# Kernel tuning notes

Hardware: AMD Instinct MI355X
Metric: run time of the kernel (lower is better)

## Reference

```python
import jax, jax.numpy as jnp
import numpy as np

B, D, K = 16384, 256, 1024

def setup_inputs() -> dict:
    key = jax.random.key(0)
    k1, k2 = jax.random.split(key)
    x = jax.random.normal(k1, (B, D), dtype=jnp.float32)
    centers = jax.random.uniform(k2, (K, D), dtype=jnp.float32)  # RandomUniform(0,1)
    betas = jnp.ones((K,), dtype=jnp.float32)
    return {"x": x, "centers": centers, "betas": betas}

def reference(x, centers, betas):
    x_sq = jnp.sum(x * x, axis=-1, keepdims=True)          # [B,1]
    c_sq = jnp.sum(centers * centers, axis=-1)             # [K]
    cross = jnp.einsum('bd,kd->bk', x, centers)            # [B,K]
    diffnorm = x_sq + c_sq[None, :] - 2.0 * cross          # [B,K]
    return jnp.exp(-betas[None, :] * diffnorm)             # [B,K]
```

## Files before the change

kernel.cpp:

```cpp
#include <hip/hip_runtime.h>
#include <stdint.h>

#define D_DIM 256
#define K_CTR 1024
#define B_ROWS 16384
#define BM 32

typedef float f32x4 __attribute__((ext_vector_type(4)));
typedef long long i64x2 __attribute__((ext_vector_type(2)));

static __device__ __forceinline__ unsigned cvt4_fp8(const float4 v) {
    int r = __builtin_amdgcn_cvt_pk_fp8_f32(v.x, v.y, 0, false);
    r = __builtin_amdgcn_cvt_pk_fp8_f32(v.z, v.w, r, true);
    return (unsigned)r;
}

__global__ __launch_bounds__(256) void rbf_prep(const float* __restrict__ centers,
                                                unsigned char* __restrict__ cbf,
                                                float* __restrict__ csq) {
    const int w = threadIdx.x >> 6;
    const int l = threadIdx.x & 63;
    const int c0 = blockIdx.x * 4 + w;
    const float4 v = *reinterpret_cast<const float4*>(centers + c0 * D_DIM + l * 4);
    float s = v.x * v.x + v.y * v.y + v.z * v.z + v.w * v.w;
    const unsigned u = cvt4_fp8(v);
    const unsigned off = (unsigned)((c0 >> 4) * 4096 + (l >> 4) * 1024
                       + (((l >> 1) & 3) * 16 + (c0 & 15)) * 16
                       + ((l >> 3) & 1) * 8 + (l & 1) * 4);
    *reinterpret_cast<unsigned*>(cbf + off) = u;
    #pragma unroll
    for (int off2 = 1; off2 < 64; off2 <<= 1) s += __shfl_xor(s, off2);
    if (l == 0) csq[c0] = s;
}

__global__ __launch_bounds__(512, 4) void rbf_main(const float* __restrict__ x,
                                                   const unsigned char* __restrict__ cbf,
                                                   const float* __restrict__ csq,
                                                   const float* __restrict__ betas,
                                                   float* __restrict__ out) {
    __shared__ __align__(16) unsigned char As[BM * D_DIM];
    __shared__ __align__(16) float obuf[2][BM * 256];
    __shared__ float xs_lds[BM];

    const int tid = threadIdx.x;
    const int w = tid >> 6;
    const int l = tid & 63;
    const int strip = (blockIdx.x & 7) * 64 + (blockIdx.x >> 3);
    const int row0 = strip * BM;

    #pragma unroll
    for (int i = 0; i < 4; ++i) {
        const int r = i * 8 + w;
        const float4 v = *reinterpret_cast<const float4*>(x + (size_t)(row0 + r) * D_DIM + l * 4);
        float s = v.x * v.x + v.y * v.y + v.z * v.z + v.w * v.w;
        const unsigned u = cvt4_fp8(v);
        const unsigned pos = (unsigned)((l >> 4) * 64 + ((l >> 1) & 3) * 16
                           + ((l >> 3) & 1) * 8 + (l & 1) * 4);
        *reinterpret_cast<unsigned*>(As + r * 256 + (pos ^ ((unsigned)(r & 7) << 4))) = u;
        #pragma unroll
        for (int off = 1; off < 64; off <<= 1) s += __shfl_xor(s, off);
        if (l == 0) xs_lds[r] = s;
    }

    const int hk = l >> 4;
    const int lr = l & 15;
    const unsigned char* bwave = cbf + l * 16;

    i64x2 b0[2][4], b1[2][4];
    {
        const unsigned char* bbase = bwave + ((w * 32) >> 4) * 4096;
        #pragma unroll
        for (int p = 0; p < 4; ++p)
            #pragma unroll
            for (int n = 0; n < 2; ++n)
                b0[n][p] = *reinterpret_cast<const i64x2*>(bbase + n * 4096 + p * 1024);
    }
    __syncthreads();

    i64x2 a[2][4];
    #pragma unroll
    for (int m = 0; m < 2; ++m) {
        const int r = m * 16 + lr;
        #pragma unroll
        for (int p = 0; p < 4; ++p)
            a[m][p] = *reinterpret_cast<const i64x2*>(
                As + r * 256 + ((unsigned)(p * 64 + hk * 16) ^ ((unsigned)(lr & 7) << 4)));
    }
    const float xs0 = xs_lds[lr];
    const float xs1 = xs_lds[16 + lr];
    const float LOG2E = 1.4426950408889634f;

    #pragma unroll
    for (int ct = 0; ct < 4; ++ct) {
        const int colq = ct * 256;
        const i64x2 (&bc)[2][4] = (ct & 1) ? b1 : b0;
        i64x2 (&bn)[2][4] = (ct & 1) ? b0 : b1;

        if (ct < 3) {
            const unsigned char* bbase = bwave + (((ct + 1) * 256 + w * 32) >> 4) * 4096;
            #pragma unroll
            for (int p = 0; p < 4; ++p)
                #pragma unroll
                for (int n = 0; n < 2; ++n)
                    bn[n][p] = *reinterpret_cast<const i64x2*>(bbase + n * 4096 + p * 1024);
        }

        f32x4 acc[2][2] = {};
        #pragma unroll
        for (int p = 0; p < 4; ++p)
            #pragma unroll
            for (int n = 0; n < 2; ++n)
                #pragma unroll
                for (int m = 0; m < 2; ++m) {
                    acc[m][n] = __builtin_amdgcn_mfma_f32_16x16x32_fp8_fp8(bc[n][p][0], a[m][p][0], acc[m][n], 0, 0, 0);
                    acc[m][n] = __builtin_amdgcn_mfma_f32_16x16x32_fp8_fp8(bc[n][p][1], a[m][p][1], acc[m][n], 0, 0, 0);
                }

        float* ob = obuf[ct & 1];
        #pragma unroll
        for (int n = 0; n < 2; ++n) {
            const int cl = w * 32 + n * 16 + hk * 4;
            const f32x4 cs = *reinterpret_cast<const f32x4*>(csq + colq + cl);
            const f32x4 bt = *reinterpret_cast<const f32x4*>(betas + colq + cl);
            f32x4 btl2, coef2, base;
            #pragma unroll
            for (int j = 0; j < 4; ++j) {
                btl2[j] = bt[j] * LOG2E;
                coef2[j] = btl2[j] + btl2[j];
                base[j] = -btl2[j] * cs[j];
            }
            #pragma unroll
            for (int m = 0; m < 2; ++m) {
                const int r = m * 16 + lr;
                const float xsv = m ? xs1 : xs0;
                f32x4 rv;
                #pragma unroll
                for (int j = 0; j < 4; ++j) {
                    const float c0 = __builtin_fmaf(-btl2[j], xsv, base[j]);
                    rv[j] = __builtin_exp2f(__builtin_fmaf(coef2[j], acc[m][n][j], c0));
                }
                *reinterpret_cast<f32x4*>(reinterpret_cast<char*>(ob)
                    + r * 1024 + ((unsigned)(cl * 4) ^ ((unsigned)(r & 7) << 4))) = rv;
            }
        }
        __syncthreads();

        #pragma unroll
        for (int i = 0; i < 4; ++i) {
            const int r = w * 4 + i;
            const f32x4 v = *reinterpret_cast<const f32x4*>(reinterpret_cast<const char*>(ob)
                    + r * 1024 + ((unsigned)(l * 16) ^ ((unsigned)(r & 7) << 4)));
            *reinterpret_cast<f32x4*>(out + (size_t)(row0 + r) * K_CTR + colq + l * 4) = v;
        }
    }
}

extern "C" void kernel_launch(void* const* d_in, const int* in_sizes, int n_in,
                              void* d_out, int out_size, void* d_ws, size_t ws_size,
                              hipStream_t stream) {
    const float* x       = (const float*)d_in[0];
    const float* centers = (const float*)d_in[1];
    const float* betas   = (const float*)d_in[2];
    float* out = (float*)d_out;

    unsigned char* cbf = (unsigned char*)d_ws;
    float* csq = (float*)((char*)d_ws + (size_t)K_CTR * D_DIM);

    rbf_prep<<<K_CTR / 4, 256, 0, stream>>>(centers, cbf, csq);
    rbf_main<<<B_ROWS / BM, 512, 0, stream>>>(x, cbf, csq, betas, out);
}
```

Measured before the change: 27.55 us.

## Fuse center prep into main kernel with grid-wide atomic barrier

Drops the separate center-preprocessing kernel. Each block of the main kernel now converts two centers to fp8 and writes their squared norms, then all blocks wait on a global atomic counter before loading B fragments. This removes one kernel launch and the gap between the two kernels, but adds a memset launch and a spin barrier that needs all 512 blocks to be co-resident. The output store loop is also split so all LDS reads are issued before the global stores.

```diff
diff --git a/kernel.cpp b/kernel.cpp
--- a/kernel.cpp
+++ b/kernel.cpp
@@ -5,6 +5,7 @@
 #define K_CTR 1024
 #define B_ROWS 16384
 #define BM 32
+#define NBLK (B_ROWS / BM)
 
 typedef float f32x4 __attribute__((ext_vector_type(4)));
 typedef long long i64x2 __attribute__((ext_vector_type(2)));
@@ -15,29 +16,11 @@
     return (unsigned)r;
 }
 
-__global__ __launch_bounds__(256) void rbf_prep(const float* __restrict__ centers,
-                                                unsigned char* __restrict__ cbf,
-                                                float* __restrict__ csq) {
-    const int w = threadIdx.x >> 6;
-    const int l = threadIdx.x & 63;
-    const int c0 = blockIdx.x * 4 + w;
-    const float4 v = *reinterpret_cast<const float4*>(centers + c0 * D_DIM + l * 4);
-    float s = v.x * v.x + v.y * v.y + v.z * v.z + v.w * v.w;
-    const unsigned u = cvt4_fp8(v);
-    const unsigned off = (unsigned)((c0 >> 4) * 4096 + (l >> 4) * 1024
-                       + (((l >> 1) & 3) * 16 + (c0 & 15)) * 16
-                       + ((l >> 3) & 1) * 8 + (l & 1) * 4);
-    *reinterpret_cast<unsigned*>(cbf + off) = u;
-    #pragma unroll
-    for (int off2 = 1; off2 < 64; off2 <<= 1) s += __shfl_xor(s, off2);
-    if (l == 0) csq[c0] = s;
-}
-
-__global__ __launch_bounds__(512, 4) void rbf_main(const float* __restrict__ x,
-                                                   const unsigned char* __restrict__ cbf,
-                                                   const float* __restrict__ csq,
-                                                   const float* __restrict__ betas,
-                                                   float* __restrict__ out) {
+__global__ __launch_bounds__(512, 4) void rbf_fused(
+        const float* __restrict__ x, const float* __restrict__ centers,
+        unsigned char* __restrict__ cbf, float* __restrict__ csq,
+        const float* __restrict__ betas, float* __restrict__ out,
+        unsigned* __restrict__ counter) {
     __shared__ __align__(16) unsigned char As[BM * D_DIM];
     __shared__ __align__(16) float obuf[2][BM * 256];
     __shared__ float xs_lds[BM];
@@ -47,6 +30,20 @@
     const int l = tid & 63;
     const int strip = (blockIdx.x & 7) * 64 + (blockIdx.x >> 3);
     const int row0 = strip * BM;
+
+    if (tid < 128) {
+        const int c0 = blockIdx.x * 2 + w;
+        const float4 v = *reinterpret_cast<const float4*>(centers + c0 * D_DIM + l * 4);
+        float s = v.x * v.x + v.y * v.y + v.z * v.z + v.w * v.w;
+        const unsigned u = cvt4_fp8(v);
+        const unsigned off = (unsigned)((c0 >> 4) * 4096 + (l >> 4) * 1024
+                           + (((l >> 1) & 3) * 16 + (c0 & 15)) * 16
+                           + ((l >> 3) & 1) * 8 + (l & 1) * 4);
+        *reinterpret_cast<unsigned*>(cbf + off) = u;
+        #pragma unroll
+        for (int off2 = 1; off2 < 64; off2 <<= 1) s += __shfl_xor(s, off2);
+        if (l == 0) csq[c0] = s;
+    }
 
     #pragma unroll
     for (int i = 0; i < 4; ++i) {
@@ -61,21 +58,19 @@
         for (int off = 1; off < 64; off <<= 1) s += __shfl_xor(s, off);
         if (l == 0) xs_lds[r] = s;
     }
+    __syncthreads();
+
+    if (tid == 0) {
+        __threadfence();
+        __hip_atomic_fetch_add(counter, 1u, __ATOMIC_RELEASE, __HIP_MEMORY_SCOPE_AGENT);
+        while (__hip_atomic_load(counter, __ATOMIC_ACQUIRE, __HIP_MEMORY_SCOPE_AGENT) < NBLK)
+            __builtin_amdgcn_s_sleep(2);
+    }
+    __syncthreads();
 
     const int hk = l >> 4;
     const int lr = l & 15;
     const unsigned char* bwave = cbf + l * 16;
-
-    i64x2 b0[2][4], b1[2][4];
-    {
-        const unsigned char* bbase = bwave + ((w * 32) >> 4) * 4096;
-        #pragma unroll
-        for (int p = 0; p < 4; ++p)
-            #pragma unroll
-            for (int n = 0; n < 2; ++n)
-                b0[n][p] = *reinterpret_cast<const i64x2*>(bbase + n * 4096 + p * 1024);
-    }
-    __syncthreads();
 
     i64x2 a[2][4];
     #pragma unroll
@@ -89,6 +84,16 @@
     const float xs0 = xs_lds[lr];
     const float xs1 = xs_lds[16 + lr];
     const float LOG2E = 1.4426950408889634f;
+
+    i64x2 b0[2][4], b1[2][4];
+    {
+        const unsigned char* bbase = bwave + ((w * 32) >> 4) * 4096;
+        #pragma unroll
+        for (int p = 0; p < 4; ++p)
+            #pragma unroll
+            for (int n = 0; n < 2; ++n)
+                b0[n][p] = *reinterpret_cast<const i64x2*>(bbase + n * 4096 + p * 1024);
+    }
 
     #pragma unroll
     for (int ct = 0; ct < 4; ++ct) {
@@ -145,12 +150,17 @@
         }
         __syncthreads();
 
+        f32x4 sv[4];
         #pragma unroll
         for (int i = 0; i < 4; ++i) {
             const int r = w * 4 + i;
-            const f32x4 v = *reinterpret_cast<const f32x4*>(reinterpret_cast<const char*>(ob)
+            sv[i] = *reinterpret_cast<const f32x4*>(reinterpret_cast<const char*>(ob)
                     + r * 1024 + ((unsigned)(l * 16) ^ ((unsigned)(r & 7) << 4)));
-            *reinterpret_cast<f32x4*>(out + (size_t)(row0 + r) * K_CTR + colq + l * 4) = v;
+        }
+        #pragma unroll
+        for (int i = 0; i < 4; ++i) {
+            const int r = w * 4 + i;
+            *reinterpret_cast<f32x4*>(out + (size_t)(row0 + r) * K_CTR + colq + l * 4) = sv[i];
         }
     }
 }
@@ -164,8 +174,9 @@
     float* out = (float*)d_out;
 
     unsigned char* cbf = (unsigned char*)d_ws;
-    float* csq = (float*)((char*)d_ws + (size_t)K_CTR * D_DIM);
+    float* csq = (float*)((char*)d_ws + 262144);
+    unsigned* counter = (unsigned*)((char*)d_ws + 262144 + 4096);
 
-    rbf_prep<<<K_CTR / 4, 256, 0, stream>>>(centers, cbf, csq);
-    rbf_main<<<B_ROWS / BM, 512, 0, stream>>>(x, cbf, csq, betas, out);
+    hipMemsetAsync(counter, 0, sizeof(unsigned), stream);
+    rbf_fused<<<NBLK, 512, 0, stream>>>(x, centers, cbf, csq, betas, out, counter);
 }
```

New measurement: 58.32 us. 2.12x slower.
